# Performance work log

Measured on AMD Instinct MI355X. Metric: run time of the kernel, lower is better.

## Reference

```python
import jax, jax.numpy as jnp
import numpy as np


def _conv1x1(x, w, b):
    # x: (B, C, H, W), w: (O, C), b: (O,) -> (B, O, H, W)
    return jnp.einsum('bchw,oc->bohw', x, w) + b[None, :, None, None]


def setup_inputs() -> dict:
    key = jax.random.key(0)
    ks = jax.random.split(key, 9)
    C, Cb = 256, 128
    B, H, W = 4, 64, 64
    s_in = 1.0 / np.sqrt(C)   # kaiming-uniform-ish scale for 1x1 convs
    s_bn = 1.0 / np.sqrt(Cb)
    return {
        'x': jax.random.normal(ks[0], (B, C, H, W), dtype=jnp.float32),
        'theta_w': jax.random.uniform(ks[1], (Cb, C), jnp.float32, -s_in, s_in),
        'theta_b': jax.random.uniform(ks[2], (Cb,), jnp.float32, -s_in, s_in),
        'phi_w': jax.random.uniform(ks[3], (Cb, C), jnp.float32, -s_in, s_in),
        'phi_b': jax.random.uniform(ks[4], (Cb,), jnp.float32, -s_in, s_in),
        'g_w': jax.random.uniform(ks[5], (Cb, C), jnp.float32, -s_in, s_in),
        'g_b': jax.random.uniform(ks[6], (Cb,), jnp.float32, -s_in, s_in),
        'W_w': jax.random.uniform(ks[7], (C, Cb), jnp.float32, -s_bn, s_bn),
        'W_b': jax.random.uniform(ks[8], (C,), jnp.float32, -s_bn, s_bn),
    }


def reference(x, theta_w, theta_b, phi_w, phi_b, g_w, g_b, W_w, W_b):
    B, C, H, Wd = x.shape
    Cb = theta_w.shape[0]
    # NOTE: the original uses raw torch.reshape (row-major), NOT transpose,
    # so (B, Cb, H, W) -> (B, H*W, Cb) scrambles channel/spatial layout.
    # We replicate that exactly with jnp.reshape.
    theta = _conv1x1(x, theta_w, theta_b).reshape(B, -1, Cb)   # (B, N, Cb)
    phi = _conv1x1(x, phi_w, phi_b).reshape(B, Cb, -1)         # (B, Cb, N)
    g = _conv1x1(x, g_w, g_b).reshape(B, -1, Cb)               # (B, N, Cb)
    scores = jnp.einsum('bnc,bcm->bnm', theta, phi)            # (B, N, N)
    attn = jax.nn.softmax(scores, axis=1)                      # softmax over dim=1 (unusual axis)
    y = jnp.einsum('bnm,bmc->bnc', attn, g)                    # (B, N, Cb)
    y = y.reshape(B, -1, H, Wd)                                # raw reshape back to (B, Cb, H, W)
    w = _conv1x1(y, W_w, W_b)                                  # (B, C, H, W)
    return w + x
```

## Files before the change

kernel.cpp:

```cpp
#include <hip/hip_runtime.h>
#include <math.h>

constexpr int CI = 256;
constexpr int CB = 128;
constexpr int HWD = 4096;
constexpr int NBATCH = 4;
constexpr int NN_ = 4096;
constexpr size_t U1 = (size_t)NBATCH * NN_ * CB;
constexpr size_t U_THETA = 0;
constexpr size_t U_PHIT  = U1;
constexpr size_t U_G     = 2 * U1;
constexpr size_t U_GT    = 3 * U1;
constexpr size_t U_Y     = 4 * U1;
constexpr size_t U_XT    = 4 * U1;
constexpr size_t U_WCAT  = 8 * U1;
constexpr size_t U_WW    = 8 * U1 + 98304;
constexpr size_t F_D     = (8 * U1 + 131072) / 2;

typedef short v8s __attribute__((ext_vector_type(8)));
typedef unsigned short u8s __attribute__((ext_vector_type(8)));
typedef float v4f __attribute__((ext_vector_type(4)));
typedef float v16f __attribute__((ext_vector_type(16)));
#define MFMA16(a, b, c) __builtin_amdgcn_mfma_f32_16x16x32_bf16(a, b, c, 0, 0, 0)
#define MFMA32(a, b, c) __builtin_amdgcn_mfma_f32_32x32x16_bf16(a, b, c, 0, 0, 0)

__device__ __forceinline__ unsigned short f2bf(float f) {
    union { float f; unsigned u; } v; v.f = f;
    unsigned r = v.u + 0x7fff + ((v.u >> 16) & 1);
    return (unsigned short)(r >> 16);
}
__device__ __forceinline__ float bf2f(unsigned short s) {
    union { unsigned u; float f; } v; v.u = (unsigned)s << 16;
    return v.f;
}

__global__ __launch_bounds__(256) void k0_xpose(
    const float* __restrict__ x, unsigned short* __restrict__ xT,
    const float* __restrict__ tw, const float* __restrict__ pw,
    const float* __restrict__ gw, const float* __restrict__ Ww,
    unsigned short* __restrict__ wcat, unsigned short* __restrict__ wwB)
{
    __shared__ unsigned short T[64 * 72];
    const int t = threadIdx.x;
    if (blockIdx.y == 4) {
        int wb = blockIdx.x + 64 * blockIdx.z;
        if (t < 128) {
            int e = (wb * 128 + t) * 4;
            const float* src; unsigned short* dst;
            if (e < 32768)       { src = tw + e;           dst = wcat + e; }
            else if (e < 65536)  { src = pw + (e - 32768); dst = wcat + e; }
            else if (e < 98304)  { src = gw + (e - 65536); dst = wcat + e; }
            else                 { src = Ww + (e - 98304); dst = wwB + (e - 98304); }
            float4 f = *(const float4*)src;
            ushort4 u;
            u.x = f2bf(f.x); u.y = f2bf(f.y); u.z = f2bf(f.z); u.w = f2bf(f.w);
            *(ushort4*)dst = u;
        }
        return;
    }
    const int hw0 = blockIdx.x * 64, c0 = blockIdx.y * 64, b = blockIdx.z;
    const float* xb = x + (size_t)b * CI * HWD;
    const int rr = t >> 4, cc = t & 15;
    #pragma unroll
    for (int pass = 0; pass < 4; pass++) {
        float4 f = *(const float4*)&xb[(size_t)(c0 + pass * 16 + rr) * HWD + hw0 + cc * 4];
        T[(cc * 4 + 0) * 72 + pass * 16 + rr] = f2bf(f.x);
        T[(cc * 4 + 1) * 72 + pass * 16 + rr] = f2bf(f.y);
        T[(cc * 4 + 2) * 72 + pass * 16 + rr] = f2bf(f.z);
        T[(cc * 4 + 3) * 72 + pass * 16 + rr] = f2bf(f.w);
    }
    __syncthreads();
    const int row = t >> 2, cs = (t & 3) * 16;
    unsigned short* dst = xT + (size_t)b * NN_ * CI;
    #pragma unroll
    for (int h = 0; h < 2; h++)
        *(u8s*)&dst[(size_t)(hw0 + row) * CI + c0 + cs + h * 8] =
            *(const u8s*)&T[row * 72 + cs + h * 8];
}

__global__ __launch_bounds__(256, 4) void k1_mfma(
    const unsigned short* __restrict__ xT, const unsigned short* __restrict__ wcat,
    const float* __restrict__ tb, const float* __restrict__ pb,
    const float* __restrict__ gb,
    unsigned short* __restrict__ thetaB, unsigned short* __restrict__ phiTB,
    unsigned short* __restrict__ gB)
{
    __shared__ unsigned short LdsX[64 * 268];
    unsigned short* T = LdsX;
    const int t = threadIdx.x;
    const int lane = t & 63, w = t >> 6;
    const int l31 = lane & 31, lh = lane >> 5;
    const int qj = w >> 1, qh = w & 1;
    const int hw0 = blockIdx.x * 64, j0 = blockIdx.y * 64, b = blockIdx.z;
    const int matId = j0 >> 7, jl0 = j0 & 127;
    const float* bvec = (matId == 0) ? tb : (matId == 1) ? pb : gb;
    const unsigned short* xb = xT + (size_t)b * NN_ * CI;

    {
        const int row = t >> 2, seg = t & 3;
        #pragma unroll
        for (int c8 = 0; c8 < 8; c8++)
            *(u8s*)&LdsX[row * 268 + seg * 64 + c8 * 8] =
                *(const u8s*)&xb[(size_t)(hw0 + row) * CI + seg * 64 + c8 * 8];
    }
    __syncthreads();

    v16f s = {};
    #pragma unroll
    for (int kt = 0; kt < 16; kt++) {
        v8s a = *(const v8s*)&wcat[(size_t)(j0 + qj * 32 + l31) * CI + kt * 16 + lh * 8];
        v8s bx = *(const v8s*)&LdsX[(qh * 32 + l31) * 268 + kt * 16 + lh * 8];
        s = MFMA32(a, bx, s);
    }

    if (matId != 1) {
        unsigned short* dst = ((matId == 0) ? thetaB : gB) + (size_t)b * CB * HWD;
        #pragma unroll
        for (int reg = 0; reg < 16; reg++) {
            int row = (reg & 3) + 8 * (reg >> 2) + 4 * lh;
            int cb = jl0 + qj * 32 + row;
            dst[(size_t)cb * HWD + hw0 + qh * 32 + l31] = f2bf(s[reg] + bvec[cb]);
        }
    } else {
        __syncthreads();
        #pragma unroll
        for (int reg = 0; reg < 16; reg++) {
            int row = (reg & 3) + 8 * (reg >> 2) + 4 * lh;
            T[(qh * 32 + l31) * 76 + qj * 32 + row] =
                f2bf(s[reg] + bvec[jl0 + qj * 32 + row]);
        }
        __syncthreads();
        unsigned short* dst = phiTB + (size_t)b * NN_ * CB;
        const int row = t >> 2, cs = (t & 3) * 16;
        #pragma unroll
        for (int h = 0; h < 2; h++)
            *(u8s*)&dst[(size_t)(hw0 + row) * CB + jl0 + cs + h * 8] =
                *(const u8s*)&T[row * 76 + cs + h * 8];
    }
}

__global__ __launch_bounds__(256, 2) void k2_colsum(
    const unsigned short* __restrict__ thetaB,
    const unsigned short* __restrict__ phiTB,
    float* __restrict__ Dout)
{
    __shared__ float part[4][128];
    const int t = threadIdx.x;
    const int lane = t & 63, w = t >> 6;
    const int ln = lane & 15, quad = lane >> 4;
    const int m0 = blockIdx.x * 128, q = blockIdx.y, b = blockIdx.z;
    const unsigned short* th = thetaB + (size_t)b * NN_ * CB;
    const unsigned short* ph = phiTB + (size_t)b * NN_ * CB;

    v8s bf[8][4];
    #pragma unroll
    for (int mt = 0; mt < 8; mt++)
        #pragma unroll
        for (int kt = 0; kt < 4; kt++)
            bf[mt][kt] = *(const v8s*)&ph[(size_t)(m0 + mt * 16 + ln) * CB + kt * 32 + quad * 8];

    float dsum[8] = {};
    const int nBeg = q * 1024 + w * 16, nEnd = q * 1024 + 1024;
    v8s af[4], afn[4];
    #pragma unroll
    for (int kt = 0; kt < 4; kt++)
        af[kt] = *(const v8s*)&th[(size_t)(nBeg + ln) * CB + kt * 32 + quad * 8];
    for (int n0 = nBeg; n0 < nEnd; n0 += 64) {
        int nn = (n0 + 64 < nEnd) ? n0 + 64 : nBeg;
        #pragma unroll
        for (int kt = 0; kt < 4; kt++)
            afn[kt] = *(const v8s*)&th[(size_t)(nn + ln) * CB + kt * 32 + quad * 8];
        #pragma unroll
        for (int mt = 0; mt < 8; mt++) {
            v4f s = {};
            #pragma unroll
            for (int kt = 0; kt < 4; kt++)
                s = MFMA16(af[kt], bf[mt][kt], s);
            #pragma unroll
            for (int r = 0; r < 4; r++)
                dsum[mt] += __expf(s[r]);
        }
        #pragma unroll
        for (int kt = 0; kt < 4; kt++) af[kt] = afn[kt];
    }
    #pragma unroll
    for (int mt = 0; mt < 8; mt++) {
        float v = dsum[mt];
        v += __shfl_xor(v, 16);
        v += __shfl_xor(v, 32);
        dsum[mt] = v;
    }
    if (quad == 0) {
        #pragma unroll
        for (int mt = 0; mt < 8; mt++) part[w][mt * 16 + ln] = dsum[mt];
    }
    __syncthreads();
    if (t < 128) {
        float v = part[0][t] + part[1][t] + part[2][t] + part[3][t];
        Dout[((size_t)q * NBATCH + b) * NN_ + m0 + t] = v;
    }
}

__global__ __launch_bounds__(256) void k1b_transpose_scale_g(
    const unsigned short* __restrict__ gB, const float* __restrict__ D,
    unsigned short* __restrict__ gTB)
{
    __shared__ unsigned short T[128 * 36];
    const int t = threadIdx.x;
    const int m0 = blockIdx.x * 32;
    const int b  = blockIdx.z;
    const unsigned short* F = gB + (size_t)b * CB * HWD;
    unsigned short* dst = gTB + (size_t)b * CB * HWD;
    const int mrow = t >> 3, cg = t & 7;
    {
        int m = m0 + mrow;
        float d = D[((size_t)0 * NBATCH + b) * NN_ + m]
                + D[((size_t)1 * NBATCH + b) * NN_ + m]
                + D[((size_t)2 * NBATCH + b) * NN_ + m]
                + D[((size_t)3 * NBATCH + b) * NN_ + m];
        float r = 1.0f / d;
        #pragma unroll
        for (int j8 = 0; j8 < 2; j8++) {
            int cbase = cg * 8 + j8 * 64;
            u8s u = *(const u8s*)&F[(size_t)m * CB + cbase];
            #pragma unroll
            for (int e = 0; e < 8; e++)
                T[(cbase + e) * 36 + mrow] = f2bf(bf2f(u[e]) * r);
        }
    }
    __syncthreads();
    const int c = t >> 1, mh = (t & 1) * 16;
    #pragma unroll
    for (int h8 = 0; h8 < 2; h8++)
        *(u8s*)&dst[(size_t)c * HWD + m0 + mh + h8 * 8] =
            *(const u8s*)&T[c * 36 + mh + h8 * 8];
}

__global__ __launch_bounds__(256, 4) void k3_attn(
    const unsigned short* __restrict__ thetaB,
    const unsigned short* __restrict__ phiTB,
    const unsigned short* __restrict__ gTB,
    unsigned short* __restrict__ Y)
{
    __shared__ unsigned short Lphi[64 * 140];
    __shared__ unsigned short Pl[64 * 76];
    const int t = threadIdx.x;
    const int lane = t & 63, w = t >> 6;
    const int l31 = lane & 31, lh = lane >> 5;
    const int qn = w & 1, qm = w >> 1;
    const int rowS = t >> 4, colS = t & 15;
    const int n0 = blockIdx.x * 64, q = blockIdx.y, b = blockIdx.z;
    const unsigned short* th = thetaB + (size_t)b * NN_ * CB;
    const unsigned short* ph = phiTB + (size_t)b * NN_ * CB;
    const unsigned short* gT = gTB + (size_t)b * CB * HWD;

    v8s ath[8];
    #pragma unroll
    for (int kt = 0; kt < 8; kt++)
        ath[kt] = *(const v8s*)&th[(size_t)(n0 + qn * 32 + l31) * CB + kt * 16 + lh * 8];

    const int mBeg = q * 1024, mEnd = mBeg + 1024;
    #pragma unroll
    for (int pass = 0; pass < 4; pass++)
        *(v8s*)&Lphi[(pass * 16 + rowS) * 140 + colS * 8] =
            *(const v8s*)&ph[(size_t)(mBeg + pass * 16 + rowS) * CB + colS * 8];
    __syncthreads();

    v16f yacc[2] = {};
    for (int m0 = mBeg; m0 < mEnd; m0 += 64) {
        int mN = (m0 + 64 < mEnd) ? m0 + 64 : mBeg;
        v8s preg[4];
        #pragma unroll
        for (int pass = 0; pass < 4; pass++)
            preg[pass] = *(const v8s*)&ph[(size_t)(mN + pass * 16 + rowS) * CB + colS * 8];
        v8s gfrag[4];
        #pragma unroll
        for (int ks = 0; ks < 4; ks++)
            gfrag[ks] = *(const v8s*)&gT[(size_t)(w * 32 + l31) * HWD + m0 + ks * 16 + lh * 8];
        v16f s = {};
        #pragma unroll
        for (int kt = 0; kt < 8; kt++) {
            v8s bphi = *(const v8s*)&Lphi[(qm * 32 + l31) * 140 + kt * 16 + lh * 8];
            s = MFMA32(ath[kt], bphi, s);
        }
        __syncthreads();
        #pragma unroll
        for (int reg = 0; reg < 16; reg++) {
            int row = qn * 32 + (reg & 3) + 8 * (reg >> 2) + 4 * lh;
            Pl[row * 76 + qm * 32 + l31] = f2bf(__expf(s[reg]));
        }
        #pragma unroll
        for (int pass = 0; pass < 4; pass++)
            *(v8s*)&Lphi[(pass * 16 + rowS) * 140 + colS * 8] = preg[pass];
        __syncthreads();
        #pragma unroll
        for (int ks = 0; ks < 4; ks++)
            #pragma unroll
            for (int nt = 0; nt < 2; nt++) {
                v8s ap = *(const v8s*)&Pl[(nt * 32 + l31) * 76 + ks * 16 + lh * 8];
                yacc[nt] = MFMA32(ap, gfrag[ks], yacc[nt]);
            }
    }
    unsigned short* yp = Y + ((size_t)q * NBATCH + b) * CB * HWD;
    #pragma unroll
    for (int nt = 0; nt < 2; nt++)
        #pragma unroll
        for (int reg = 0; reg < 16; reg++) {
            int row = (reg & 3) + 8 * (reg >> 2) + 4 * lh;
            yp[(size_t)(n0 + nt * 32 + row) * CB + w * 32 + l31] = f2bf(yacc[nt][reg]);
        }
}

__global__ __launch_bounds__(256, 2) void k4_mfma(
    const float* __restrict__ x, const unsigned short* __restrict__ wwB,
    const float* __restrict__ Wb, const unsigned short* __restrict__ Ybuf,
    float* __restrict__ out)
{
    __shared__ unsigned short Yt[64 * 136];
    const int t = threadIdx.x;
    const int lane = t & 63, w = t >> 6;
    const int ln = lane & 15, quad = lane >> 4;
    const int hw0 = blockIdx.x * 64, o0 = blockIdx.y * 128, b = blockIdx.z;

    const int cb = t >> 1, seg = (t & 1) * 32;
    #pragma unroll
    for (int g8 = 0; g8 < 4; g8++) {
        float sum[8] = {};
        #pragma unroll
        for (int q = 0; q < 4; q++) {
            u8s u = *(const u8s*)&Ybuf[((size_t)q * NBATCH + b) * CB * HWD +
                                       (size_t)cb * HWD + hw0 + seg + g8 * 8];
            #pragma unroll
            for (int j = 0; j < 8; j++) sum[j] += bf2f(u[j]);
        }
        #pragma unroll
        for (int j = 0; j < 8; j++)
            Yt[(seg + g8 * 8 + j) * 136 + cb] = f2bf(sum[j]);
    }
    __syncthreads();

    v8s aw[2][4];
    #pragma unroll
    for (int os = 0; os < 2; os++)
        #pragma unroll
        for (int kt = 0; kt < 4; kt++)
            aw[os][kt] = *(const v8s*)&wwB[(size_t)(o0 + w * 32 + os * 16 + ln) * CB + kt * 32 + quad * 8];

    v4f s[2][4] = {};
    #pragma unroll
    for (int kt = 0; kt < 4; kt++) {
        v8s by[4];
        #pragma unroll
        for (int mt = 0; mt < 4; mt++)
            by[mt] = *(const v8s*)&Yt[(mt * 16 + ln) * 136 + kt * 32 + quad * 8];
        #pragma unroll
        for (int os = 0; os < 2; os++)
            #pragma unroll
            for (int mt = 0; mt < 4; mt++)
                s[os][mt] = MFMA16(aw[os][kt], by[mt], s[os][mt]);
    }
    #pragma unroll
    for (int os = 0; os < 2; os++)
        #pragma unroll
        for (int mt = 0; mt < 4; mt++)
            #pragma unroll
            for (int r = 0; r < 4; r++) {
                int o = o0 + w * 32 + os * 16 + quad * 4 + r;
                size_t idx = (size_t)b * CI * HWD + (size_t)o * HWD + hw0 + mt * 16 + ln;
                out[idx] = s[os][mt][r] + Wb[o] + x[idx];
            }
}

extern "C" void kernel_launch(void* const* d_in, const int* in_sizes, int n_in,
                              void* d_out, int out_size, void* d_ws, size_t ws_size,
                              hipStream_t stream)
{
    const float* x  = (const float*)d_in[0];
    const float* tw = (const float*)d_in[1];
    const float* tb = (const float*)d_in[2];
    const float* pw = (const float*)d_in[3];
    const float* pb = (const float*)d_in[4];
    const float* gw = (const float*)d_in[5];
    const float* gb = (const float*)d_in[6];
    const float* Ww = (const float*)d_in[7];
    const float* Wb = (const float*)d_in[8];
    unsigned short* wsu = (unsigned short*)d_ws;
    float* wsf = (float*)d_ws;
    unsigned short* thetaB = wsu + U_THETA;
    unsigned short* phiTB  = wsu + U_PHIT;
    unsigned short* gB     = wsu + U_G;
    unsigned short* gTB    = wsu + U_GT;
    unsigned short* Ybuf   = wsu + U_Y;
    unsigned short* xTB    = wsu + U_XT;
    unsigned short* wcatB  = wsu + U_WCAT;
    unsigned short* wwB    = wsu + U_WW;
    float* Dbuf = wsf + F_D;
    float* out = (float*)d_out;
    dim3 blk(256, 1, 1);
    hipLaunchKernelGGL(k0_xpose, dim3(64, 5, NBATCH), blk, 0, stream,
                       x, xTB, tw, pw, gw, Ww, wcatB, wwB);
    hipLaunchKernelGGL(k1_mfma, dim3(64, 6, NBATCH), blk, 0, stream,
                       xTB, wcatB, tb, pb, gb, thetaB, phiTB, gB);
    hipLaunchKernelGGL(k2_colsum, dim3(32, 4, NBATCH), blk, 0, stream,
                       thetaB, phiTB, Dbuf);
    hipLaunchKernelGGL(k1b_transpose_scale_g, dim3(128, 1, NBATCH), blk, 0, stream,
                       gB, Dbuf, gTB);
    hipLaunchKernelGGL(k3_attn, dim3(64, 4, NBATCH), blk, 0, stream,
                       thetaB, phiTB, gTB, Ybuf);
    hipLaunchKernelGGL(k4_mfma, dim3(64, 2, NBATCH), blk, 0, stream,
                       x, wwB, Wb, Ybuf, out);
}
```

Baseline: 194.8 us.

## Double-buffer phi and P tiles in attention kernel to drop a barrier

The attention kernel now keeps two LDS buffers each for the phi tile and the probability tile. This lets each iteration write the next phi tile and the current P tile before a single __syncthreads instead of two, and issues the global prefetch two tiles ahead. The intent is to remove one block-wide barrier per iteration and hide more global load latency. In exchange it uses more LDS, changes the padding strides (140→132, 76→68, which may add bank conflicts) and lowers the launch-bounds occupancy hint from 4 to 3.

```diff
diff --git a/kernel.cpp b/kernel.cpp
--- a/kernel.cpp
+++ b/kernel.cpp
@@ -236,14 +236,14 @@
             *(const u8s*)&T[c * 36 + mh + h8 * 8];
 }
 
-__global__ __launch_bounds__(256, 4) void k3_attn(
+__global__ __launch_bounds__(256, 3) void k3_attn(
     const unsigned short* __restrict__ thetaB,
     const unsigned short* __restrict__ phiTB,
     const unsigned short* __restrict__ gTB,
     unsigned short* __restrict__ Y)
 {
-    __shared__ unsigned short Lphi[64 * 140];
-    __shared__ unsigned short Pl[64 * 76];
+    __shared__ unsigned short Lphi[2][64 * 132];
+    __shared__ unsigned short Pl[2][64 * 68];
     const int t = threadIdx.x;
     const int lane = t & 63, w = t >> 6;
     const int l31 = lane & 31, lh = lane >> 5;
@@ -259,20 +259,24 @@
     for (int kt = 0; kt < 8; kt++)
         ath[kt] = *(const v8s*)&th[(size_t)(n0 + qn * 32 + l31) * CB + kt * 16 + lh * 8];
 
-    const int mBeg = q * 1024, mEnd = mBeg + 1024;
+    const int mBeg = q * 1024;
+    v8s preg[4];
     #pragma unroll
     for (int pass = 0; pass < 4; pass++)
-        *(v8s*)&Lphi[(pass * 16 + rowS) * 140 + colS * 8] =
-            *(const v8s*)&ph[(size_t)(mBeg + pass * 16 + rowS) * CB + colS * 8];
+        preg[pass] = *(const v8s*)&ph[(size_t)(mBeg + pass * 16 + rowS) * CB + colS * 8];
+    #pragma unroll
+    for (int pass = 0; pass < 4; pass++)
+        *(v8s*)&Lphi[0][(pass * 16 + rowS) * 132 + colS * 8] = preg[pass];
+    #pragma unroll
+    for (int pass = 0; pass < 4; pass++)
+        preg[pass] = *(const v8s*)&ph[(size_t)(mBeg + 64 + pass * 16 + rowS) * CB + colS * 8];
     __syncthreads();
 
     v16f yacc[2] = {};
-    for (int m0 = mBeg; m0 < mEnd; m0 += 64) {
-        int mN = (m0 + 64 < mEnd) ? m0 + 64 : mBeg;
-        v8s preg[4];
-        #pragma unroll
-        for (int pass = 0; pass < 4; pass++)
-            preg[pass] = *(const v8s*)&ph[(size_t)(mN + pass * 16 + rowS) * CB + colS * 8];
+    #pragma unroll 2
+    for (int it = 0; it < 16; ++it) {
+        const int cur = it & 1;
+        const int m0 = mBeg + it * 64;
         v8s gfrag[4];
         #pragma unroll
         for (int ks = 0; ks < 4; ks++)
@@ -280,24 +284,27 @@
         v16f s = {};
         #pragma unroll
         for (int kt = 0; kt < 8; kt++) {
-            v8s bphi = *(const v8s*)&Lphi[(qm * 32 + l31) * 140 + kt * 16 + lh * 8];
+            v8s bphi = *(const v8s*)&Lphi[cur][(qm * 32 + l31) * 132 + kt * 16 + lh * 8];
             s = MFMA32(ath[kt], bphi, s);
         }
-        __syncthreads();
+        #pragma unroll
+        for (int pass = 0; pass < 4; pass++)
+            *(v8s*)&Lphi[cur ^ 1][(pass * 16 + rowS) * 132 + colS * 8] = preg[pass];
         #pragma unroll
         for (int reg = 0; reg < 16; reg++) {
             int row = qn * 32 + (reg & 3) + 8 * (reg >> 2) + 4 * lh;
-            Pl[row * 76 + qm * 32 + l31] = f2bf(__expf(s[reg]));
-        }
+            Pl[cur][row * 68 + qm * 32 + l31] = f2bf(__expf(s[reg]));
+        }
+        __syncthreads();
+        const int mP = mBeg + ((it + 2) & 15) * 64;
         #pragma unroll
         for (int pass = 0; pass < 4; pass++)
-            *(v8s*)&Lphi[(pass * 16 + rowS) * 140 + colS * 8] = preg[pass];
-        __syncthreads();
+            preg[pass] = *(const v8s*)&ph[(size_t)(mP + pass * 16 + rowS) * CB + colS * 8];
         #pragma unroll
         for (int ks = 0; ks < 4; ks++)
             #pragma unroll
             for (int nt = 0; nt < 2; nt++) {
-                v8s ap = *(const v8s*)&Pl[(nt * 32 + l31) * 76 + ks * 16 + lh * 8];
+                v8s ap = *(const v8s*)&Pl[cur][(nt * 32 + l31) * 68 + ks * 16 + lh * 8];
                 yacc[nt] = MFMA32(ap, gfrag[ks], yacc[nt]);
             }
     }
```

Measured after the change: 196.3 us. No clear change (+0.7%).

## Restructure column-sum kernel with 32x32 MFMA and LDS-staged theta tiles

Applied to the files above, without the earlier changes.

The softmax denominator kernel now works on 64-column tiles with 32x32x16 MFMA instead of 16x16x32. Each 64-row theta tile is staged in padded shared memory and shared by all four waves, while the next tile is prefetched into registers. The grid is doubled and occupancy raised to 4 blocks per SM to cut per-wave register pressure and repeated global theta loads. In exchange it adds two block-wide barriers per iteration and uses more LDS per block.

```diff
diff --git a/kernel.cpp b/kernel.cpp
--- a/kernel.cpp
+++ b/kernel.cpp
@@ -139,65 +139,63 @@
     }
 }
 
-__global__ __launch_bounds__(256, 2) void k2_colsum(
+__global__ __launch_bounds__(256, 4) void k2_colsum(
     const unsigned short* __restrict__ thetaB,
     const unsigned short* __restrict__ phiTB,
     float* __restrict__ Dout)
 {
-    __shared__ float part[4][128];
+    __shared__ unsigned short Lth[64 * 140];
+    __shared__ float part[4][32];
     const int t = threadIdx.x;
     const int lane = t & 63, w = t >> 6;
-    const int ln = lane & 15, quad = lane >> 4;
-    const int m0 = blockIdx.x * 128, q = blockIdx.y, b = blockIdx.z;
+    const int l31 = lane & 31, lh = lane >> 5;
+    const int qn = w & 1, qm = w >> 1;
+    const int rowS = t >> 4, colS = t & 15;
+    const int m0 = blockIdx.x * 64, q = blockIdx.y, b = blockIdx.z;
     const unsigned short* th = thetaB + (size_t)b * NN_ * CB;
     const unsigned short* ph = phiTB + (size_t)b * NN_ * CB;
 
-    v8s bf[8][4];
-    #pragma unroll
-    for (int mt = 0; mt < 8; mt++)
-        #pragma unroll
-        for (int kt = 0; kt < 4; kt++)
-            bf[mt][kt] = *(const v8s*)&ph[(size_t)(m0 + mt * 16 + ln) * CB + kt * 32 + quad * 8];
-
-    float dsum[8] = {};
-    const int nBeg = q * 1024 + w * 16, nEnd = q * 1024 + 1024;
-    v8s af[4], afn[4];
-    #pragma unroll
-    for (int kt = 0; kt < 4; kt++)
-        af[kt] = *(const v8s*)&th[(size_t)(nBeg + ln) * CB + kt * 32 + quad * 8];
+    v8s bphi[8];
+    #pragma unroll
+    for (int kt = 0; kt < 8; kt++)
+        bphi[kt] = *(const v8s*)&ph[(size_t)(m0 + qm * 32 + l31) * CB + kt * 16 + lh * 8];
+
+    const int nBeg = q * 1024, nEnd = nBeg + 1024;
+    #pragma unroll
+    for (int pass = 0; pass < 4; pass++)
+        *(v8s*)&Lth[(pass * 16 + rowS) * 140 + colS * 8] =
+            *(const v8s*)&th[(size_t)(nBeg + pass * 16 + rowS) * CB + colS * 8];
+    __syncthreads();
+
+    float dsum = 0.f;
     for (int n0 = nBeg; n0 < nEnd; n0 += 64) {
-        int nn = (n0 + 64 < nEnd) ? n0 + 64 : nBeg;
-        #pragma unroll
-        for (int kt = 0; kt < 4; kt++)
-            afn[kt] = *(const v8s*)&th[(size_t)(nn + ln) * CB + kt * 32 + quad * 8];
-        #pragma unroll
-        for (int mt = 0; mt < 8; mt++) {
-            v4f s = {};
-            #pragma unroll
-            for (int kt = 0; kt < 4; kt++)
-                s = MFMA16(af[kt], bf[mt][kt], s);
-            #pragma unroll
-            for (int r = 0; r < 4; r++)
-                dsum[mt] += __expf(s[r]);
-        }
-        #pragma unroll
-        for (int kt = 0; kt < 4; kt++) af[kt] = afn[kt];
-    }
-    #pragma unroll
-    for (int mt = 0; mt < 8; mt++) {
-        float v = dsum[mt];
-        v += __shfl_xor(v, 16);
-        v += __shfl_xor(v, 32);
-        dsum[mt] = v;
-    }
-    if (quad == 0) {
-        #pragma unroll
-        for (int mt = 0; mt < 8; mt++) part[w][mt * 16 + ln] = dsum[mt];
-    }
-    __syncthreads();
-    if (t < 128) {
-        float v = part[0][t] + part[1][t] + part[2][t] + part[3][t];
-        Dout[((size_t)q * NBATCH + b) * NN_ + m0 + t] = v;
+        int nN = (n0 + 64 < nEnd) ? n0 + 64 : nBeg;
+        v8s preg[4];
+        #pragma unroll
+        for (int pass = 0; pass < 4; pass++)
+            preg[pass] = *(const v8s*)&th[(size_t)(nN + pass * 16 + rowS) * CB + colS * 8];
+        v16f s = {};
+        #pragma unroll
+        for (int kt = 0; kt < 8; kt++) {
+            v8s ath = *(const v8s*)&Lth[(qn * 32 + l31) * 140 + kt * 16 + lh * 8];
+            s = MFMA32(ath, bphi[kt], s);
+        }
+        __syncthreads();
+        #pragma unroll
+        for (int pass = 0; pass < 4; pass++)
+            *(v8s*)&Lth[(pass * 16 + rowS) * 140 + colS * 8] = preg[pass];
+        __syncthreads();
+        #pragma unroll
+        for (int reg = 0; reg < 16; reg++)
+            dsum += __expf(s[reg]);
+    }
+    dsum += __shfl_xor(dsum, 32);
+    if (lane < 32) part[w][l31] = dsum;
+    __syncthreads();
+    if (t < 64) {
+        int qmIdx = t >> 5, j = t & 31;
+        float v = part[qmIdx * 2 + 0][j] + part[qmIdx * 2 + 1][j];
+        Dout[((size_t)q * NBATCH + b) * NN_ + m0 + qmIdx * 32 + j] = v;
     }
 }
 
@@ -401,7 +399,7 @@
                        x, xTB, tw, pw, gw, Ww, wcatB, wwB);
     hipLaunchKernelGGL(k1_mfma, dim3(64, 6, NBATCH), blk, 0, stream,
                        xTB, wcatB, tb, pb, gb, thetaB, phiTB, gB);
-    hipLaunchKernelGGL(k2_colsum, dim3(32, 4, NBATCH), blk, 0, stream,
+    hipLaunchKernelGGL(k2_colsum, dim3(64, 4, NBATCH), blk, 0, stream,
                        thetaB, phiTB, Dbuf);
     hipLaunchKernelGGL(k1b_transpose_scale_g, dim3(128, 1, NBATCH), blk, 0, stream,
                        gB, Dbuf, gTB);
```

Result: no change. 195.0 us (+0.1%).
